# Optimization experiments

Hardware: AMD Instinct MI355X
Metric: run time of the kernel (lower is better)

Reference implementation:

```python
import jax, jax.numpy as jnp
import numpy as np

N_NODES = 100000


def _gcn_norm(edge_index, n):
    # Add self loops and compute symmetric normalization deg^-1/2 A_hat deg^-1/2
    loops = jnp.arange(n, dtype=edge_index.dtype)
    row = jnp.concatenate([edge_index[0], loops])  # source nodes [E+N]
    col = jnp.concatenate([edge_index[1], loops])  # target nodes [E+N]
    ones = jnp.ones(row.shape[0], dtype=jnp.float32)
    deg = jax.ops.segment_sum(ones, col, num_segments=n)  # in-degree incl. self loop
    dinv = jnp.where(deg > 0, jax.lax.rsqrt(deg), 0.0)
    norm = dinv[row] * dinv[col]  # [E+N]
    return row, col, norm


def _gcn_conv(x, W, b, row, col, norm, n):
    h = x @ W                     # [N, out]
    msg = h[row] * norm[:, None]  # gather + scale  [E+N, out]
    agg = jax.ops.segment_sum(msg, col, num_segments=n)  # scatter-add
    return agg + b


def setup_inputs() -> dict:
    key = jax.random.key(0)
    ks = jax.random.split(key, 8)
    n, e, din, dh, dout = N_NODES, 1600000, 128, 128, 64
    x = jax.random.normal(ks[0], (n, din), dtype=jnp.float32)
    edge_index = jax.random.randint(ks[1], (2, e), 0, n, dtype=jnp.int64)
    s = lambda fan: 1.0 / np.sqrt(fan)
    W0 = jax.random.normal(ks[2], (din, dh), dtype=jnp.float32) * s(din)
    W1 = jax.random.normal(ks[3], (dh, dh), dtype=jnp.float32) * s(dh)
    W2 = jax.random.normal(ks[4], (dh, dout), dtype=jnp.float32) * s(dh)
    b0 = jnp.zeros((dh,), jnp.float32)
    b1 = jnp.zeros((dh,), jnp.float32)
    b2 = jnp.zeros((dout,), jnp.float32)
    return {"x": x, "edge_index": edge_index, "W0": W0, "b0": b0,
            "W1": W1, "b1": b1, "W2": W2, "b2": b2}


def reference(x, edge_index, W0, b0, W1, b1, W2, b2):
    # Eval-mode forward (dropout inactive), matching GCN.forward
    n = x.shape[0]
    row, col, norm = _gcn_norm(edge_index, n)
    h = jax.nn.relu(_gcn_conv(x, W0, b0, row, col, norm, n))
    h = jax.nn.relu(_gcn_conv(h, W1, b1, row, col, norm, n))
    out = _gcn_conv(h, W2, b2, row, col, norm, n)
    return out
```

## Files before the change

### kernel.cpp

```cpp
#include <hip/hip_runtime.h>
#include <stdint.h>


static inline size_t ws_align(size_t x) { return (x + 255) & ~(size_t)255; }

#define SRCM 0x1FFFFu

typedef float __f2 __attribute__((ext_vector_type(2)));

__device__ __forceinline__ int eidx(const void* p, size_t i, int is64) {
  return is64 ? (int)((const long long*)p)[i] : ((const int*)p)[i];
}

__device__ __forceinline__ uint16_t f2bf(float f) {
  uint32_t u = __float_as_uint(f);
  u += 0x7fffu + ((u >> 16) & 1u);
  return (uint16_t)(u >> 16);
}
__device__ __forceinline__ float bf_lo(uint32_t h) { return __uint_as_float(h << 16); }
__device__ __forceinline__ float bf_hi(uint32_t h) { return __uint_as_float(h & 0xffff0000u); }

__global__ void detect_k(const int* ei, int* flag) {
  if (threadIdx.x == 0 && blockIdx.x == 0) {
    int allz = 1;
    for (int i = 1; i < 128; i += 2)
      if (ei[i] != 0) { allz = 0; break; }
    *flag = allz;
  }
}

__global__ __launch_bounds__(256) void passA_k(const void* ei, const int* __restrict__ flag,
                                               int* __restrict__ bucket_cnt, int E, int NB) {
  __shared__ int cnt[256];
  int t = threadIdx.x;
  cnt[t] = 0;
  __syncthreads();
  int is64 = *flag;
  for (int e = blockIdx.x * 256 + t; e < E; e += gridDim.x * 256) {
    int c = eidx(ei, (size_t)E + e, is64);
    atomicAdd(&cnt[c >> 9], 1);
  }
  __syncthreads();
  if (t < NB && cnt[t]) atomicAdd(&bucket_cnt[t], cnt[t]);
}

__global__ __launch_bounds__(256) void bscan_k(const int* __restrict__ bucket_cnt,
                                               int* __restrict__ bucket_offs,
                                               int* __restrict__ gcursor, int NB) {
  __shared__ int sh[256];
  int t = threadIdx.x;
  int v = (t < NB) ? bucket_cnt[t] : 0;
  sh[t] = v;
  __syncthreads();
  for (int off = 1; off < 256; off <<= 1) {
    int x = (t >= off) ? sh[t - off] : 0;
    __syncthreads();
    sh[t] += x;
    __syncthreads();
  }
  if (t < NB) {
    int excl = sh[t] - v;
    bucket_offs[t] = excl;
    gcursor[t] = excl;
  }
  if (t == NB - 1) bucket_offs[NB] = sh[t];
}

__global__ __launch_bounds__(256) void passB_k(const void* ei, const int* __restrict__ flag,
                                               int* __restrict__ gcursor,
                                               int2* __restrict__ epk_binned, int E, int NB) {
  __shared__ int2 sorted[4096];
  __shared__ int cnt[256], bbase[256], gb[256], cur[256];
  const int t = threadIdx.x;
  const int base = blockIdx.x * 4096;
  const int CH = min(4096, E - base);
  const int is64 = *flag;

  cnt[t] = 0;
  __syncthreads();
  for (int i = t; i < CH; i += 256) {
    int c = eidx(ei, (size_t)E + base + i, is64);
    atomicAdd(&cnt[c >> 9], 1);
  }
  __syncthreads();
  {
    int v = cnt[t];
    __shared__ int sh[256];
    sh[t] = v;
    __syncthreads();
    for (int off = 1; off < 256; off <<= 1) {
      int x = (t >= off) ? sh[t - off] : 0;
      __syncthreads();
      sh[t] += x;
      __syncthreads();
    }
    bbase[t] = sh[t] - v;
    gb[t] = (t < NB && v) ? atomicAdd(&gcursor[t], v) : 0;
    cur[t] = 0;
  }
  __syncthreads();
  for (int i = t; i < CH; i += 256) {
    int r = eidx(ei, (size_t)base + i, is64);
    int c = eidx(ei, (size_t)E + base + i, is64);
    int b = c >> 9;
    int rank = atomicAdd(&cur[b], 1);
    sorted[bbase[b] + rank] = make_int2(r, c);
  }
  __syncthreads();
  for (int i = t; i < CH; i += 256) {
    int2 v = sorted[i];
    int b = v.y >> 9;
    epk_binned[gb[b] + (i - bbase[b])] = v;
  }
}

__global__ __launch_bounds__(256) void passC0_k(const int2* __restrict__ epk_binned,
                                                const int* __restrict__ bucket_offs,
                                                int* __restrict__ deg, int* __restrict__ offs,
                                                int n, int NB) {
  __shared__ int dcnt[512];
  __shared__ int s[256];
  const int t = threadIdx.x;
  const int b = blockIdx.x;
  dcnt[t] = 0; dcnt[t + 256] = 0;
  __syncthreads();
  const int lo = bucket_offs[b], hi = bucket_offs[b + 1];
  for (int i = lo + t; i < hi; i += 256)
    atomicAdd(&dcnt[epk_binned[i].y & 511], 1);
  __syncthreads();
  int d0 = dcnt[2 * t], d1 = dcnt[2 * t + 1];
  int pv = d0 + d1;
  s[t] = pv;
  __syncthreads();
  for (int off = 1; off < 256; off <<= 1) {
    int x = (t >= off) ? s[t - off] : 0;
    __syncthreads();
    s[t] += x;
    __syncthreads();
  }
  int pex = s[t] - pv;
  const int node0 = b << 9;
  int g0 = node0 + 2 * t, g1 = node0 + 2 * t + 1;
  if (g0 < n) { deg[g0] = d0; offs[g0] = lo + pex; }
  if (g1 < n) { deg[g1] = d1; offs[g1] = lo + pex + d0; }
  if (b == NB - 1 && t == 0) offs[n] = hi;
}

__global__ void dinv_k(const int* __restrict__ deg, float* __restrict__ dinv, int n) {
  int i = blockIdx.x * blockDim.x + threadIdx.x;
  if (i < n) dinv[i] = rsqrtf((float)deg[i] + 1.0f);
}

__global__ __launch_bounds__(256) void passC_k(const int2* __restrict__ epk_binned,
                                               const int* __restrict__ bucket_offs,
                                               const int* __restrict__ offs,
                                               uint32_t* __restrict__ epk) {
  __shared__ int cur[512];
  const int t = threadIdx.x;
  const int b = blockIdx.x;
  cur[t] = 0; cur[t + 256] = 0;
  __syncthreads();
  const int lo = bucket_offs[b], hi = bucket_offs[b + 1];
  for (int i = lo + t; i < hi; i += 256) {
    int2 v = epk_binned[i];
    int pos = offs[v.y] + atomicAdd(&cur[v.y & 511], 1);
    epk[pos] = (uint32_t)v.x;
  }
}

template <int COLS, bool SLICED_IN>
__global__ __launch_bounds__(256) void gemm_k(const float* __restrict__ X,
                                              const float* __restrict__ W,
                                              const float* __restrict__ dinv,
                                              uint16_t* __restrict__ H, int N) {
  constexpr int KB = 32;
  constexpr int CG = COLS / 8;
  constexpr int RG = 256 / CG;
  constexpr int ROWS = RG * 8;
  constexpr int XP = ROWS + 4;

  __shared__ float Xs[KB][XP];
  __shared__ float Ws[KB][COLS];

  const int tid = threadIdx.x;
  const int cg = tid % CG, rg = tid / CG;
  const int c0 = cg * 8, rr0 = rg * 8;
  const int rowbase = blockIdx.x * ROWS;
  const float4* X4 = (const float4*)X;

  float acc[8][8];
#pragma unroll
  for (int a = 0; a < 8; ++a)
#pragma unroll
    for (int b = 0; b < 8; ++b) acc[a][b] = 0.f;

  for (int k0 = 0; k0 < 128; k0 += KB) {
    __syncthreads();
#pragma unroll
    for (int i = tid; i < KB * (COLS / 4); i += 256) {
      int kk = i / (COLS / 4);
      int cc = i % (COLS / 4);
      float4 w = ((const float4*)(W + (size_t)(k0 + kk) * COLS))[cc];
      ((float4*)&Ws[kk][0])[cc] = w;
    }
#pragma unroll
    for (int i = tid; i < ROWS * (KB / 4); i += 256) {
      int rr = i / (KB / 4);
      int k4 = i % (KB / 4);
      int gr = rowbase + rr;
      if (gr >= N) gr = N - 1;
      float4 xv;
      if (SLICED_IN) {
        int k = k0 + k4 * 4;
        int s = k >> 4, q = (k & 15) >> 2;
        xv = X4[((size_t)s * N + gr) * 4 + q];
      } else {
        xv = X4[(size_t)gr * 32 + (k0 >> 2) + k4];
      }
      Xs[k4 * 4 + 0][rr] = xv.x;
      Xs[k4 * 4 + 1][rr] = xv.y;
      Xs[k4 * 4 + 2][rr] = xv.z;
      Xs[k4 * 4 + 3][rr] = xv.w;
    }
    __syncthreads();
#pragma unroll 2
    for (int k = 0; k < KB; ++k) {
      float4 xa = *(const float4*)&Xs[k][rr0];
      float4 xb = *(const float4*)&Xs[k][rr0 + 4];
      float4 wa = *(const float4*)&Ws[k][c0];
      float4 wb = *(const float4*)&Ws[k][c0 + 4];
      float xr[8] = {xa.x, xa.y, xa.z, xa.w, xb.x, xb.y, xb.z, xb.w};
      float wr[8] = {wa.x, wa.y, wa.z, wa.w, wb.x, wb.y, wb.z, wb.w};
#pragma unroll
      for (int a = 0; a < 8; ++a)
#pragma unroll
        for (int b = 0; b < 8; ++b) acc[a][b] = fmaf(xr[a], wr[b], acc[a][b]);
    }
  }
  uint32_t* HW = (uint32_t*)H;
  const int wbase = c0 >> 1;
  const int sl = wbase >> 3;
  const int woff = wbase & 7;
#pragma unroll
  for (int a = 0; a < 8; ++a) {
    int row = rowbase + rr0 + a;
    if (row < N) {
      float sc = dinv[row];
      uint32_t p[4];
#pragma unroll
      for (int q = 0; q < 4; ++q)
        p[q] = (uint32_t)f2bf(sc * acc[a][2 * q]) | ((uint32_t)f2bf(sc * acc[a][2 * q + 1]) << 16);
      uint4 ov = make_uint4(p[0], p[1], p[2], p[3]);
      *(uint4*)&HW[((size_t)sl * N + row) * 8 + woff] = ov;
    }
  }
}

__global__ __launch_bounds__(256) void agg128s_k(const uint32_t* __restrict__ HW,
                                                 const int* __restrict__ offs,
                                                 const uint32_t* __restrict__ epk,
                                                 const float* __restrict__ bias,
                                                 float* __restrict__ Aout,
                                                 int relu, int N) {
  const int s = blockIdx.x & 7;
  const int g = blockIdx.x >> 3;
  const int lane = threadIdx.x & 63;
  const int wid = threadIdx.x >> 6;
  const int d = lane >> 3, w = lane & 7;
  const int c = g * 32 + wid * 8 + d;
  if (c >= N) return;
  const uint32_t* Hs = HW + (size_t)s * N * 8;
  int e0 = offs[c], e1 = offs[c + 1];
  float ax = 0.f, ay = 0.f;
  int e = e0;
  for (; e + 8 <= e1; e += 8) {
    uint32_t p0 = epk[e],     p1 = epk[e + 1], p2 = epk[e + 2], p3 = epk[e + 3];
    uint32_t p4 = epk[e + 4], p5 = epk[e + 5], p6 = epk[e + 6], p7 = epk[e + 7];
    uint32_t h0 = Hs[(size_t)p0 * 8 + w];
    uint32_t h1 = Hs[(size_t)p1 * 8 + w];
    uint32_t h2 = Hs[(size_t)p2 * 8 + w];
    uint32_t h3 = Hs[(size_t)p3 * 8 + w];
    uint32_t h4 = Hs[(size_t)p4 * 8 + w];
    uint32_t h5 = Hs[(size_t)p5 * 8 + w];
    uint32_t h6 = Hs[(size_t)p6 * 8 + w];
    uint32_t h7 = Hs[(size_t)p7 * 8 + w];
    ax += bf_lo(h0); ay += bf_hi(h0);
    ax += bf_lo(h1); ay += bf_hi(h1);
    ax += bf_lo(h2); ay += bf_hi(h2);
    ax += bf_lo(h3); ay += bf_hi(h3);
    ax += bf_lo(h4); ay += bf_hi(h4);
    ax += bf_lo(h5); ay += bf_hi(h5);
    ax += bf_lo(h6); ay += bf_hi(h6);
    ax += bf_lo(h7); ay += bf_hi(h7);
  }
  for (; e + 4 <= e1; e += 4) {
    uint32_t p0 = epk[e], p1 = epk[e + 1], p2 = epk[e + 2], p3 = epk[e + 3];
    uint32_t h0 = Hs[(size_t)p0 * 8 + w];
    uint32_t h1 = Hs[(size_t)p1 * 8 + w];
    uint32_t h2 = Hs[(size_t)p2 * 8 + w];
    uint32_t h3 = Hs[(size_t)p3 * 8 + w];
    ax += bf_lo(h0); ay += bf_hi(h0);
    ax += bf_lo(h1); ay += bf_hi(h1);
    ax += bf_lo(h2); ay += bf_hi(h2);
    ax += bf_lo(h3); ay += bf_hi(h3);
  }
  for (; e < e1; ++e) {
    uint32_t h = Hs[(size_t)epk[e] * 8 + w];
    ax += bf_lo(h); ay += bf_hi(h);
  }
  float dc = rsqrtf((float)(e1 - e0) + 1.f);
  uint32_t hc = Hs[(size_t)c * 8 + w];
  float rx = fmaf(dc, ax + bf_lo(hc), bias[s * 16 + 2 * w]);
  float ry = fmaf(dc, ay + bf_hi(hc), bias[s * 16 + 2 * w + 1]);
  if (relu) { rx = fmaxf(rx, 0.f); ry = fmaxf(ry, 0.f); }
  __f2 res; res.x = rx; res.y = ry;
  __builtin_nontemporal_store(res, (__f2*)(Aout + ((size_t)s * N + c) * 16) + w);
}

__global__ __launch_bounds__(256) void agg64s_k(const uint32_t* __restrict__ HW,
                                                const int* __restrict__ offs,
                                                const uint32_t* __restrict__ epk,
                                                const float* __restrict__ bias,
                                                float* __restrict__ out, int N) {
  const int r = blockIdx.x & 7;
  const int s = r >> 1;
  const int half = r & 1;
  const int ng = (N + 31) >> 5;
  const int nh = (ng + 1) >> 1;
  const int g = half * nh + (blockIdx.x >> 3);
  if (g >= ng) return;
  const int lane = threadIdx.x & 63;
  const int wid = threadIdx.x >> 6;
  const int d = lane >> 3, w = lane & 7;
  const int c = g * 32 + wid * 8 + d;
  if (c >= N) return;
  const uint32_t* Hs = HW + (size_t)s * N * 8;
  int e0 = offs[c], e1 = offs[c + 1];
  float ax = 0.f, ay = 0.f;
  int e = e0;
  for (; e + 8 <= e1; e += 8) {
    uint32_t p0 = epk[e],     p1 = epk[e + 1], p2 = epk[e + 2], p3 = epk[e + 3];
    uint32_t p4 = epk[e + 4], p5 = epk[e + 5], p6 = epk[e + 6], p7 = epk[e + 7];
    uint32_t h0 = Hs[(size_t)p0 * 8 + w];
    uint32_t h1 = Hs[(size_t)p1 * 8 + w];
    uint32_t h2 = Hs[(size_t)p2 * 8 + w];
    uint32_t h3 = Hs[(size_t)p3 * 8 + w];
    uint32_t h4 = Hs[(size_t)p4 * 8 + w];
    uint32_t h5 = Hs[(size_t)p5 * 8 + w];
    uint32_t h6 = Hs[(size_t)p6 * 8 + w];
    uint32_t h7 = Hs[(size_t)p7 * 8 + w];
    ax += bf_lo(h0); ay += bf_hi(h0);
    ax += bf_lo(h1); ay += bf_hi(h1);
    ax += bf_lo(h2); ay += bf_hi(h2);
    ax += bf_lo(h3); ay += bf_hi(h3);
    ax += bf_lo(h4); ay += bf_hi(h4);
    ax += bf_lo(h5); ay += bf_hi(h5);
    ax += bf_lo(h6); ay += bf_hi(h6);
    ax += bf_lo(h7); ay += bf_hi(h7);
  }
  for (; e + 4 <= e1; e += 4) {
    uint32_t p0 = epk[e], p1 = epk[e + 1], p2 = epk[e + 2], p3 = epk[e + 3];
    uint32_t h0 = Hs[(size_t)p0 * 8 + w];
    uint32_t h1 = Hs[(size_t)p1 * 8 + w];
    uint32_t h2 = Hs[(size_t)p2 * 8 + w];
    uint32_t h3 = Hs[(size_t)p3 * 8 + w];
    ax += bf_lo(h0); ay += bf_hi(h0);
    ax += bf_lo(h1); ay += bf_hi(h1);
    ax += bf_lo(h2); ay += bf_hi(h2);
    ax += bf_lo(h3); ay += bf_hi(h3);
  }
  for (; e < e1; ++e) {
    uint32_t h = Hs[(size_t)epk[e] * 8 + w];
    ax += bf_lo(h); ay += bf_hi(h);
  }
  float dc = rsqrtf((float)(e1 - e0) + 1.f);
  uint32_t hc = Hs[(size_t)c * 8 + w];
  float rx = fmaf(dc, ax + bf_lo(hc), bias[s * 16 + 2 * w]);
  float ry = fmaf(dc, ay + bf_hi(hc), bias[s * 16 + 2 * w + 1]);
  __f2 res; res.x = rx; res.y = ry;
  __builtin_nontemporal_store(res, (__f2*)(out + (size_t)c * 64) + s * 8 + w);
}

extern "C" void kernel_launch(void* const* d_in, const int* in_sizes, int n_in,
                              void* d_out, int out_size, void* d_ws, size_t ws_size,
                              hipStream_t stream) {
  const float* x  = (const float*)d_in[0];
  const void*  ei = d_in[1];
  const float* W0 = (const float*)d_in[2];
  const float* b0 = (const float*)d_in[3];
  const float* W1 = (const float*)d_in[4];
  const float* b1 = (const float*)d_in[5];
  const float* W2 = (const float*)d_in[6];
  const float* b2 = (const float*)d_in[7];
  float* out = (float*)d_out;

  const int n = in_sizes[0] / 128;
  const int E = in_sizes[1] / 2;
  const int NB = (n + 511) >> 9;

  char* ws = (char*)d_ws;
  size_t off = 0;
  auto alloc = [&](size_t bytes) { char* p = ws + off; off = ws_align(off + bytes); return p; };
  int*      bucket_cnt  = (int*)alloc(256 * 4);
  int*      bucket_offs = (int*)alloc(257 * 4);
  int*      gcursor     = (int*)alloc(256 * 4);
  int*      deg         = (int*)alloc((size_t)n * 4);
  int*      offs        = (int*)alloc((size_t)(n + 1) * 4);
  float*    dinv        = (float*)alloc((size_t)n * 4);
  int*      flag        = (int*)alloc(4);
  int2*     epk_binned  = (int2*)alloc((size_t)E * 8);
  uint32_t* epk         = (uint32_t*)alloc((size_t)E * 4);
  uint16_t* hbuf        = (uint16_t*)alloc((size_t)n * 128 * 2);
  float*    abuf        = (float*)alloc((size_t)n * 128 * 4);
  (void)ws_size;

  hipMemsetAsync(bucket_cnt, 0, 256 * 4, stream);

  detect_k<<<1, 64, 0, stream>>>((const int*)ei, flag);
  passA_k<<<512, 256, 0, stream>>>(ei, flag, bucket_cnt, E, NB);
  bscan_k<<<1, 256, 0, stream>>>(bucket_cnt, bucket_offs, gcursor, NB);
  passB_k<<<(E + 4095) / 4096, 256, 0, stream>>>(ei, flag, gcursor, epk_binned, E, NB);
  passC0_k<<<NB, 256, 0, stream>>>(epk_binned, bucket_offs, deg, offs, n, NB);
  dinv_k<<<(n + 255) / 256, 256, 0, stream>>>(deg, dinv, n);
  passC_k<<<NB, 256, 0, stream>>>(epk_binned, bucket_offs, offs, epk);

  const int agg128_blocks = 8 * ((n + 31) / 32);
  const int ng = (n + 31) >> 5, nh = (ng + 1) >> 1;
  const int agg64_blocks = 8 * nh;

  gemm_k<128, false><<<(n + 127) / 128, 256, 0, stream>>>(x, W0, dinv, hbuf, n);
  agg128s_k<<<agg128_blocks, 256, 0, stream>>>((const uint32_t*)hbuf, offs, epk, b0, abuf, 1, n);
  gemm_k<128, true><<<(n + 127) / 128, 256, 0, stream>>>(abuf, W1, dinv, hbuf, n);
  agg128s_k<<<agg128_blocks, 256, 0, stream>>>((const uint32_t*)hbuf, offs, epk, b1, abuf, 1, n);
  gemm_k<64, true><<<(n + 255) / 256, 256, 0, stream>>>(abuf, W2, dinv, hbuf, n);
  agg64s_k<<<agg64_blocks, 256, 0, stream>>>((const uint32_t*)hbuf, offs, epk, b2, out, n);
}
```

Measured before the change: 521.3 us.

## Widen feature slices from 16 to 32 columns in gather-aggregate layout

Changes the sliced intermediate layout so each slice holds 32 features (64 bytes in bf16) instead of 16, and updates the GEMM writer, the GEMM sliced reader and both aggregation kernels to match. Each lane now gathers a uint2 (4 bf16) per edge and stores a float4, so there are half as many slice passes over the edge list. This halves the repeated reads of offsets and edge indices and gives each random gather a wider access. In exchange the per-slice working set doubles, which may lower cache hit rate on the gathered rows, and launch_bounds now requests 8 blocks per CU.

```diff
diff --git a/kernel.cpp b/kernel.cpp
--- a/kernel.cpp
+++ b/kernel.cpp
@@ -4,9 +4,8 @@
 
 static inline size_t ws_align(size_t x) { return (x + 255) & ~(size_t)255; }
 
-#define SRCM 0x1FFFFu
-
 typedef float __f2 __attribute__((ext_vector_type(2)));
+typedef float __f4 __attribute__((ext_vector_type(4)));
 
 __device__ __forceinline__ int eidx(const void* p, size_t i, int is64) {
   return is64 ? (int)((const long long*)p)[i] : ((const int*)p)[i];
@@ -212,8 +211,8 @@
       float4 xv;
       if (SLICED_IN) {
         int k = k0 + k4 * 4;
-        int s = k >> 4, q = (k & 15) >> 2;
-        xv = X4[((size_t)s * N + gr) * 4 + q];
+        int s = k >> 5, q = (k & 31) >> 2;
+        xv = X4[((size_t)s * N + gr) * 8 + q];
       } else {
         xv = X4[(size_t)gr * 32 + (k0 >> 2) + k4];
       }
@@ -239,8 +238,8 @@
   }
   uint32_t* HW = (uint32_t*)H;
   const int wbase = c0 >> 1;
-  const int sl = wbase >> 3;
-  const int woff = wbase & 7;
+  const int sl = wbase >> 4;
+  const int woff = wbase & 15;
 #pragma unroll
   for (int a = 0; a < 8; ++a) {
     int row = rowbase + rr0 + a;
@@ -251,134 +250,141 @@
       for (int q = 0; q < 4; ++q)
         p[q] = (uint32_t)f2bf(sc * acc[a][2 * q]) | ((uint32_t)f2bf(sc * acc[a][2 * q + 1]) << 16);
       uint4 ov = make_uint4(p[0], p[1], p[2], p[3]);
-      *(uint4*)&HW[((size_t)sl * N + row) * 8 + woff] = ov;
+      *(uint4*)&HW[((size_t)sl * N + row) * 16 + woff] = ov;
     }
   }
 }
 
-__global__ __launch_bounds__(256) void agg128s_k(const uint32_t* __restrict__ HW,
-                                                 const int* __restrict__ offs,
-                                                 const uint32_t* __restrict__ epk,
-                                                 const float* __restrict__ bias,
-                                                 float* __restrict__ Aout,
-                                                 int relu, int N) {
-  const int s = blockIdx.x & 7;
-  const int g = blockIdx.x >> 3;
+__global__ __launch_bounds__(256, 8) void agg128s_k(const uint32_t* __restrict__ HW,
+                                                    const int* __restrict__ offs,
+                                                    const uint32_t* __restrict__ epk,
+                                                    const float* __restrict__ bias,
+                                                    float* __restrict__ Aout,
+                                                    int relu, int N) {
+  const int s = blockIdx.x & 3;
+  const int g = blockIdx.x >> 2;
   const int lane = threadIdx.x & 63;
   const int wid = threadIdx.x >> 6;
   const int d = lane >> 3, w = lane & 7;
   const int c = g * 32 + wid * 8 + d;
   if (c >= N) return;
-  const uint32_t* Hs = HW + (size_t)s * N * 8;
+  const uint32_t* Hs = HW + (size_t)s * N * 16;
   int e0 = offs[c], e1 = offs[c + 1];
-  float ax = 0.f, ay = 0.f;
+  float a0 = 0.f, a1 = 0.f, a2 = 0.f, a3 = 0.f;
   int e = e0;
   for (; e + 8 <= e1; e += 8) {
     uint32_t p0 = epk[e],     p1 = epk[e + 1], p2 = epk[e + 2], p3 = epk[e + 3];
     uint32_t p4 = epk[e + 4], p5 = epk[e + 5], p6 = epk[e + 6], p7 = epk[e + 7];
-    uint32_t h0 = Hs[(size_t)p0 * 8 + w];
-    uint32_t h1 = Hs[(size_t)p1 * 8 + w];
-    uint32_t h2 = Hs[(size_t)p2 * 8 + w];
-    uint32_t h3 = Hs[(size_t)p3 * 8 + w];
-    uint32_t h4 = Hs[(size_t)p4 * 8 + w];
-    uint32_t h5 = Hs[(size_t)p5 * 8 + w];
-    uint32_t h6 = Hs[(size_t)p6 * 8 + w];
-    uint32_t h7 = Hs[(size_t)p7 * 8 + w];
-    ax += bf_lo(h0); ay += bf_hi(h0);
-    ax += bf_lo(h1); ay += bf_hi(h1);
-    ax += bf_lo(h2); ay += bf_hi(h2);
-    ax += bf_lo(h3); ay += bf_hi(h3);
-    ax += bf_lo(h4); ay += bf_hi(h4);
-    ax += bf_lo(h5); ay += bf_hi(h5);
-    ax += bf_lo(h6); ay += bf_hi(h6);
-    ax += bf_lo(h7); ay += bf_hi(h7);
+    uint2 h0 = *(const uint2*)&Hs[(size_t)p0 * 16 + 2 * w];
+    uint2 h1 = *(const uint2*)&Hs[(size_t)p1 * 16 + 2 * w];
+    uint2 h2 = *(const uint2*)&Hs[(size_t)p2 * 16 + 2 * w];
+    uint2 h3 = *(const uint2*)&Hs[(size_t)p3 * 16 + 2 * w];
+    uint2 h4 = *(const uint2*)&Hs[(size_t)p4 * 16 + 2 * w];
+    uint2 h5 = *(const uint2*)&Hs[(size_t)p5 * 16 + 2 * w];
+    uint2 h6 = *(const uint2*)&Hs[(size_t)p6 * 16 + 2 * w];
+    uint2 h7 = *(const uint2*)&Hs[(size_t)p7 * 16 + 2 * w];
+    a0 += bf_lo(h0.x); a1 += bf_hi(h0.x); a2 += bf_lo(h0.y); a3 += bf_hi(h0.y);
+    a0 += bf_lo(h1.x); a1 += bf_hi(h1.x); a2 += bf_lo(h1.y); a3 += bf_hi(h1.y);
+    a0 += bf_lo(h2.x); a1 += bf_hi(h2.x); a2 += bf_lo(h2.y); a3 += bf_hi(h2.y);
+    a0 += bf_lo(h3.x); a1 += bf_hi(h3.x); a2 += bf_lo(h3.y); a3 += bf_hi(h3.y);
+    a0 += bf_lo(h4.x); a1 += bf_hi(h4.x); a2 += bf_lo(h4.y); a3 += bf_hi(h4.y);
+    a0 += bf_lo(h5.x); a1 += bf_hi(h5.x); a2 += bf_lo(h5.y); a3 += bf_hi(h5.y);
+    a0 += bf_lo(h6.x); a1 += bf_hi(h6.x); a2 += bf_lo(h6.y); a3 += bf_hi(h6.y);
+    a0 += bf_lo(h7.x); a1 += bf_hi(h7.x); a2 += bf_lo(h7.y); a3 += bf_hi(h7.y);
   }
   for (; e + 4 <= e1; e += 4) {
     uint32_t p0 = epk[e], p1 = epk[e + 1], p2 = epk[e + 2], p3 = epk[e + 3];
-    uint32_t h0 = Hs[(size_t)p0 * 8 + w];
-    uint32_t h1 = Hs[(size_t)p1 * 8 + w];
-    uint32_t h2 = Hs[(size_t)p2 * 8 + w];
-    uint32_t h3 = Hs[(size_t)p3 * 8 + w];
-    ax += bf_lo(h0); ay += bf_hi(h0);
-    ax += bf_lo(h1); ay += bf_hi(h1);
-    ax += bf_lo(h2); ay += bf_hi(h2);
-    ax += bf_lo(h3); ay += bf_hi(h3);
+    uint2 h0 = *(const uint2*)&Hs[(size_t)p0 * 16 + 2 * w];
+    uint2 h1 = *(const uint2*)&Hs[(size_t)p1 * 16 + 2 * w];
+    uint2 h2 = *(const uint2*)&Hs[(size_t)p2 * 16 + 2 * w];
+    uint2 h3 = *(const uint2*)&Hs[(size_t)p3 * 16 + 2 * w];
+    a0 += bf_lo(h0.x); a1 += bf_hi(h0.x); a2 += bf_lo(h0.y); a3 += bf_hi(h0.y);
+    a0 += bf_lo(h1.x); a1 += bf_hi(h1.x); a2 += bf_lo(h1.y); a3 += bf_hi(h1.y);
+    a0 += bf_lo(h2.x); a1 += bf_hi(h2.x); a2 += bf_lo(h2.y); a3 += bf_hi(h2.y);
+    a0 += bf_lo(h3.x); a1 += bf_hi(h3.x); a2 += bf_lo(h3.y); a3 += bf_hi(h3.y);
   }
   for (; e < e1; ++e) {
-    uint32_t h = Hs[(size_t)epk[e] * 8 + w];
-    ax += bf_lo(h); ay += bf_hi(h);
+    uint2 h = *(const uint2*)&Hs[(size_t)epk[e] * 16 + 2 * w];
+    a0 += bf_lo(h.x); a1 += bf_hi(h.x); a2 += bf_lo(h.y); a3 += bf_hi(h.y);
   }
   float dc = rsqrtf((float)(e1 - e0) + 1.f);
-  uint32_t hc = Hs[(size_t)c * 8 + w];
-  float rx = fmaf(dc, ax + bf_lo(hc), bias[s * 16 + 2 * w]);
-  float ry = fmaf(dc, ay + bf_hi(hc), bias[s * 16 + 2 * w + 1]);
-  if (relu) { rx = fmaxf(rx, 0.f); ry = fmaxf(ry, 0.f); }
-  __f2 res; res.x = rx; res.y = ry;
-  __builtin_nontemporal_store(res, (__f2*)(Aout + ((size_t)s * N + c) * 16) + w);
-}
-
-__global__ __launch_bounds__(256) void agg64s_k(const uint32_t* __restrict__ HW,
-                                                const int* __restrict__ offs,
-                                                const uint32_t* __restrict__ epk,
-                                                const float* __restrict__ bias,
-                                                float* __restrict__ out, int N) {
+  uint2 hc = *(const uint2*)&Hs[(size_t)c * 16 + 2 * w];
+  float r0 = fmaf(dc, a0 + bf_lo(hc.x), bias[s * 32 + 4 * w + 0]);
+  float r1 = fmaf(dc, a1 + bf_hi(hc.x), bias[s * 32 + 4 * w + 1]);
+  float r2 = fmaf(dc, a2 + bf_lo(hc.y), bias[s * 32 + 4 * w + 2]);
+  float r3 = fmaf(dc, a3 + bf_hi(hc.y), bias[s * 32 + 4 * w + 3]);
+  if (relu) {
+    r0 = fmaxf(r0, 0.f); r1 = fmaxf(r1, 0.f);
+    r2 = fmaxf(r2, 0.f); r3 = fmaxf(r3, 0.f);
+  }
+  __f4 res; res.x = r0; res.y = r1; res.z = r2; res.w = r3;
+  __builtin_nontemporal_store(res, (__f4*)(Aout + ((size_t)s * N + c) * 32 + 4 * w));
+}
+
+__global__ __launch_bounds__(256, 8) void agg64s_k(const uint32_t* __restrict__ HW,
+                                                   const int* __restrict__ offs,
+                                                   const uint32_t* __restrict__ epk,
+                                                   const float* __restrict__ bias,
+                                                   float* __restrict__ out, int N) {
   const int r = blockIdx.x & 7;
-  const int s = r >> 1;
-  const int half = r & 1;
+  const int s = r >> 2;
+  const int quar = r & 3;
   const int ng = (N + 31) >> 5;
-  const int nh = (ng + 1) >> 1;
-  const int g = half * nh + (blockIdx.x >> 3);
+  const int nq = (ng + 3) >> 2;
+  const int g = quar * nq + (blockIdx.x >> 3);
   if (g >= ng) return;
   const int lane = threadIdx.x & 63;
   const int wid = threadIdx.x >> 6;
   const int d = lane >> 3, w = lane & 7;
   const int c = g * 32 + wid * 8 + d;
   if (c >= N) return;
-  const uint32_t* Hs = HW + (size_t)s * N * 8;
+  const uint32_t* Hs = HW + (size_t)s * N * 16;
   int e0 = offs[c], e1 = offs[c + 1];
-  float ax = 0.f, ay = 0.f;
+  float a0 = 0.f, a1 = 0.f, a2 = 0.f, a3 = 0.f;
   int e = e0;
   for (; e + 8 <= e1; e += 8) {
     uint32_t p0 = epk[e],     p1 = epk[e + 1], p2 = epk[e + 2], p3 = epk[e + 3];
     uint32_t p4 = epk[e + 4], p5 = epk[e + 5], p6 = epk[e + 6], p7 = epk[e + 7];
-    uint32_t h0 = Hs[(size_t)p0 * 8 + w];
-    uint32_t h1 = Hs[(size_t)p1 * 8 + w];
-    uint32_t h2 = Hs[(size_t)p2 * 8 + w];
-    uint32_t h3 = Hs[(size_t)p3 * 8 + w];
-    uint32_t h4 = Hs[(size_t)p4 * 8 + w];
-    uint32_t h5 = Hs[(size_t)p5 * 8 + w];
-    uint32_t h6 = Hs[(size_t)p6 * 8 + w];
-    uint32_t h7 = Hs[(size_t)p7 * 8 + w];
-    ax += bf_lo(h0); ay += bf_hi(h0);
-    ax += bf_lo(h1); ay += bf_hi(h1);
-    ax += bf_lo(h2); ay += bf_hi(h2);
-    ax += bf_lo(h3); ay += bf_hi(h3);
-    ax += bf_lo(h4); ay += bf_hi(h4);
-    ax += bf_lo(h5); ay += bf_hi(h5);
-    ax += bf_lo(h6); ay += bf_hi(h6);
-    ax += bf_lo(h7); ay += bf_hi(h7);
+    uint2 h0 = *(const uint2*)&Hs[(size_t)p0 * 16 + 2 * w];
+    uint2 h1 = *(const uint2*)&Hs[(size_t)p1 * 16 + 2 * w];
+    uint2 h2 = *(const uint2*)&Hs[(size_t)p2 * 16 + 2 * w];
+    uint2 h3 = *(const uint2*)&Hs[(size_t)p3 * 16 + 2 * w];
+    uint2 h4 = *(const uint2*)&Hs[(size_t)p4 * 16 + 2 * w];
+    uint2 h5 = *(const uint2*)&Hs[(size_t)p5 * 16 + 2 * w];
+    uint2 h6 = *(const uint2*)&Hs[(size_t)p6 * 16 + 2 * w];
+    uint2 h7 = *(const uint2*)&Hs[(size_t)p7 * 16 + 2 * w];
+    a0 += bf_lo(h0.x); a1 += bf_hi(h0.x); a2 += bf_lo(h0.y); a3 += bf_hi(h0.y);
+    a0 += bf_lo(h1.x); a1 += bf_hi(h1.x); a2 += bf_lo(h1.y); a3 += bf_hi(h1.y);
+    a0 += bf_lo(h2.x); a1 += bf_hi(h2.x); a2 += bf_lo(h2.y); a3 += bf_hi(h2.y);
+    a0 += bf_lo(h3.x); a1 += bf_hi(h3.x); a2 += bf_lo(h3.y); a3 += bf_hi(h3.y);
+    a0 += bf_lo(h4.x); a1 += bf_hi(h4.x); a2 += bf_lo(h4.y); a3 += bf_hi(h4.y);
+    a0 += bf_lo(h5.x); a1 += bf_hi(h5.x); a2 += bf_lo(h5.y); a3 += bf_hi(h5.y);
+    a0 += bf_lo(h6.x); a1 += bf_hi(h6.x); a2 += bf_lo(h6.y); a3 += bf_hi(h6.y);
+    a0 += bf_lo(h7.x); a1 += bf_hi(h7.x); a2 += bf_lo(h7.y); a3 += bf_hi(h7.y);
   }
   for (; e + 4 <= e1; e += 4) {
     uint32_t p0 = epk[e], p1 = epk[e + 1], p2 = epk[e + 2], p3 = epk[e + 3];
-    uint32_t h0 = Hs[(size_t)p0 * 8 + w];
-    uint32_t h1 = Hs[(size_t)p1 * 8 + w];
-    uint32_t h2 = Hs[(size_t)p2 * 8 + w];
-    uint32_t h3 = Hs[(size_t)p3 * 8 + w];
-    ax += bf_lo(h0); ay += bf_hi(h0);
-    ax += bf_lo(h1); ay += bf_hi(h1);
-    ax += bf_lo(h2); ay += bf_hi(h2);
-    ax += bf_lo(h3); ay += bf_hi(h3);
+    uint2 h0 = *(const uint2*)&Hs[(size_t)p0 * 16 + 2 * w];
+    uint2 h1 = *(const uint2*)&Hs[(size_t)p1 * 16 + 2 * w];
+    uint2 h2 = *(const uint2*)&Hs[(size_t)p2 * 16 + 2 * w];
+    uint2 h3 = *(const uint2*)&Hs[(size_t)p3 * 16 + 2 * w];
+    a0 += bf_lo(h0.x); a1 += bf_hi(h0.x); a2 += bf_lo(h0.y); a3 += bf_hi(h0.y);
+    a0 += bf_lo(h1.x); a1 += bf_hi(h1.x); a2 += bf_lo(h1.y); a3 += bf_hi(h1.y);
+    a0 += bf_lo(h2.x); a1 += bf_hi(h2.x); a2 += bf_lo(h2.y); a3 += bf_hi(h2.y);
+    a0 += bf_lo(h3.x); a1 += bf_hi(h3.x); a2 += bf_lo(h3.y); a3 += bf_hi(h3.y);
   }
   for (; e < e1; ++e) {
-    uint32_t h = Hs[(size_t)epk[e] * 8 + w];
-    ax += bf_lo(h); ay += bf_hi(h);
+    uint2 h = *(const uint2*)&Hs[(size_t)epk[e] * 16 + 2 * w];
+    a0 += bf_lo(h.x); a1 += bf_hi(h.x); a2 += bf_lo(h.y); a3 += bf_hi(h.y);
   }
   float dc = rsqrtf((float)(e1 - e0) + 1.f);
-  uint32_t hc = Hs[(size_t)c * 8 + w];
-  float rx = fmaf(dc, ax + bf_lo(hc), bias[s * 16 + 2 * w]);
-  float ry = fmaf(dc, ay + bf_hi(hc), bias[s * 16 + 2 * w + 1]);
-  __f2 res; res.x = rx; res.y = ry;
-  __builtin_nontemporal_store(res, (__f2*)(out + (size_t)c * 64) + s * 8 + w);
+  uint2 hc = *(const uint2*)&Hs[(size_t)c * 16 + 2 * w];
+  float r0 = fmaf(dc, a0 + bf_lo(hc.x), bias[s * 32 + 4 * w + 0]);
+  float r1 = fmaf(dc, a1 + bf_hi(hc.x), bias[s * 32 + 4 * w + 1]);
+  float r2 = fmaf(dc, a2 + bf_lo(hc.y), bias[s * 32 + 4 * w + 2]);
+  float r3 = fmaf(dc, a3 + bf_hi(hc.y), bias[s * 32 + 4 * w + 3]);
+  __f4 res; res.x = r0; res.y = r1; res.z = r2; res.w = r3;
+  __builtin_nontemporal_store(res, (__f4*)(out + (size_t)c * 64 + s * 32 + 4 * w));
 }
 
 extern "C" void kernel_launch(void* const* d_in, const int* in_sizes, int n_in,
@@ -424,9 +430,9 @@
   dinv_k<<<(n + 255) / 256, 256, 0, stream>>>(deg, dinv, n);
   passC_k<<<NB, 256, 0, stream>>>(epk_binned, bucket_offs, offs, epk);
 
-  const int agg128_blocks = 8 * ((n + 31) / 32);
-  const int ng = (n + 31) >> 5, nh = (ng + 1) >> 1;
-  const int agg64_blocks = 8 * nh;
+  const int agg128_blocks = 4 * ((n + 31) / 32);
+  const int ng = (n + 31) >> 5, nq = (ng + 3) >> 2;
+  const int agg64_blocks = 8 * nq;
 
   gemm_k<128, false><<<(n + 127) / 128, 256, 0, stream>>>(x, W0, dinv, hbuf, n);
   agg128s_k<<<agg128_blocks, 256, 0, stream>>>((const uint32_t*)hbuf, offs, epk, b0, abuf, 1, n);
```

Result: faster. 497.0 us (-4.7%).
